# Kernel tuning notes

Hardware: AMD Instinct MI355X
Metric: run time of the kernel (lower is better)

The kernel has to match this reference:

```python
import jax, jax.numpy as jnp
import numpy as np

B, N_TOK, DIM, HEADS, FRAMES = 16, 1569, 768, 12, 8
HEAD_DIM = DIM // HEADS
N_SPACE = (N_TOK - 1) // FRAMES  # 196
EPS = 1e-6


def _ln(x, w, b):
    m = jnp.mean(x, axis=-1, keepdims=True)
    v = jnp.var(x, axis=-1, keepdims=True)
    return (x - m) * jax.lax.rsqrt(v + EPS) * w + b


def _sdpa(q, k, v):
    # q: [..., Sq, d], k/v: [..., Sk, d]
    s = jnp.einsum('...qd,...kd->...qk', q, k) * (HEAD_DIM ** -0.5)
    return jnp.einsum('...qk,...kd->...qd', jax.nn.softmax(s, axis=-1), v)


def _divided_attn(x, w_qkv, b_qkv, w_proj, b_proj, mode):
    # Faithful translation of DividedAttention.forward
    Bb, N, D = x.shape
    h, d, f = HEADS, HEAD_DIM, FRAMES
    n = (N - 1) // f
    qkv = x @ w_qkv + b_qkv                      # [B, N, 3D]
    q, k, v = jnp.split(qkv, 3, axis=-1)
    q, k, v = (t.reshape(Bb, N, h, d).transpose(0, 2, 1, 3) for t in (q, k, v))  # [B,h,N,d]
    # global cls-token attention over ALL tokens
    cls_out = _sdpa(q[:, :, :1], k, v)           # [B,h,1,d]
    # local tokens: split (f n) per einops pattern 'b (f n) d'
    q_, k_, v_ = (t[:, :, 1:].reshape(Bb, h, f, n, d) for t in (q, k, v))
    if mode == 'time':
        # '(b n) f d': batch over spatial positions, attend over frames
        q_, k_, v_ = (t.transpose(0, 1, 3, 2, 4) for t in (q_, k_, v_))  # [B,h,n,f,d]
        r = n
    else:
        # '(b f) n d': batch over frames, attend over spatial positions
        r = f
    cls_k = jnp.broadcast_to(k[:, :, None, :1], (Bb, h, r, 1, d))
    cls_v = jnp.broadcast_to(v[:, :, None, :1], (Bb, h, r, 1, d))
    out = _sdpa(q_,
                jnp.concatenate([cls_k, k_], axis=3),
                jnp.concatenate([cls_v, v_], axis=3))   # [B,h,r,seq,d]
    if mode == 'time':
        out = out.transpose(0, 1, 3, 2, 4)       # back to [B,h,f,n,d]
    out = out.reshape(Bb, h, N - 1, d)
    out = jnp.concatenate([cls_out, out], axis=2)          # [B,h,N,d]
    out = out.transpose(0, 2, 1, 3).reshape(Bb, N, D)      # 'b n (h d)'
    return out @ w_proj + b_proj


def setup_inputs() -> dict:
    key = jax.random.key(0)
    ks = jax.random.split(key, 8)
    s = 0.02
    return {
        'x': jax.random.normal(ks[0], (B, N_TOK, DIM), jnp.float32),
        'norm1_w': jnp.ones((DIM,), jnp.float32),
        'norm1_b': jnp.zeros((DIM,), jnp.float32),
        'norm2_w': jnp.ones((DIM,), jnp.float32),
        'norm2_b': jnp.zeros((DIM,), jnp.float32),
        'norm3_w': jnp.ones((DIM,), jnp.float32),
        'norm3_b': jnp.zeros((DIM,), jnp.float32),
        'time_qkv_w': jax.random.normal(ks[1], (DIM, 3 * DIM), jnp.float32) * s,
        'time_qkv_b': jnp.zeros((3 * DIM,), jnp.float32),
        'time_proj_w': jax.random.normal(ks[2], (DIM, DIM), jnp.float32) * s,
        'time_proj_b': jnp.zeros((DIM,), jnp.float32),
        'space_qkv_w': jax.random.normal(ks[3], (DIM, 3 * DIM), jnp.float32) * s,
        'space_qkv_b': jnp.zeros((3 * DIM,), jnp.float32),
        'space_proj_w': jax.random.normal(ks[4], (DIM, DIM), jnp.float32) * s,
        'space_proj_b': jnp.zeros((DIM,), jnp.float32),
        'mlp_w1': jax.random.normal(ks[5], (DIM, 4 * DIM), jnp.float32) * s,
        'mlp_b1': jnp.zeros((4 * DIM,), jnp.float32),
        'mlp_w2': jax.random.normal(ks[6], (4 * DIM, DIM), jnp.float32) * s,
        'mlp_b2': jnp.zeros((DIM,), jnp.float32),
    }


def reference(x, norm1_w, norm1_b, norm2_w, norm2_b, norm3_w, norm3_b,
              time_qkv_w, time_qkv_b, time_proj_w, time_proj_b,
              space_qkv_w, space_qkv_b, space_proj_w, space_proj_b,
              mlp_w1, mlp_b1, mlp_w2, mlp_b2):
    # DividedSpaceTimeBlock.forward
    t = _divided_attn(_ln(x, norm3_w, norm3_b),
                      time_qkv_w, time_qkv_b, time_proj_w, time_proj_b, 'time')
    x = x + t
    s = _divided_attn(_ln(x, norm1_w, norm1_b),
                      space_qkv_w, space_qkv_b, space_proj_w, space_proj_b, 'space')
    x = x + s
    h = jax.nn.gelu(_ln(x, norm2_w, norm2_b) @ mlp_w1 + mlp_b1)
    return x + h @ mlp_w2 + mlp_b2
```

## Files before the change

kernel.cpp:

```cpp
#include <hip/hip_runtime.h>
#include <cstdint>
#include <cstddef>

typedef unsigned short u16;
typedef __attribute__((ext_vector_type(8))) short short8;
typedef __attribute__((ext_vector_type(4))) float f32x4;

#define BB 16
#define NT 1569
#define DIM 768
#define NH 12
#define HD 64
#define FR 8
#define NS 196
#define MROWS (BB*NT)
#define NKEY 197

__device__ __forceinline__ float bf2f(u16 h) {
    return __uint_as_float(((unsigned int)h) << 16);
}
__device__ __forceinline__ u16 f2bf(float f) {
    unsigned int u = __float_as_uint(f);
    u += 0x7fff + ((u >> 16) & 1);
    return (u16)(u >> 16);
}

__global__ __launch_bounds__(256) void ln_kernel(const float* __restrict__ x,
        const float* __restrict__ w, const float* __restrict__ b,
        u16* __restrict__ out) {
    int row = blockIdx.x;
    size_t base = (size_t)row * DIM;
    int tid = threadIdx.x;
    float v0 = x[base + tid];
    float v1 = x[base + tid + 256];
    float v2 = x[base + tid + 512];
    float s = v0 + v1 + v2;
    float q = v0*v0 + v1*v1 + v2*v2;
    #pragma unroll
    for (int o = 32; o >= 1; o >>= 1) {
        s += __shfl_xor(s, o, 64);
        q += __shfl_xor(q, o, 64);
    }
    __shared__ float rs[4], rq[4];
    int wave = tid >> 6, lane = tid & 63;
    if (lane == 0) { rs[wave] = s; rq[wave] = q; }
    __syncthreads();
    float S = rs[0]+rs[1]+rs[2]+rs[3];
    float Q = rq[0]+rq[1]+rq[2]+rq[3];
    float mean = S * (1.0f/DIM);
    float var  = Q * (1.0f/DIM) - mean*mean;
    float inv  = rsqrtf(var + 1e-6f);
    out[base+tid]     = f2bf((v0-mean)*inv*w[tid]     + b[tid]);
    out[base+tid+256] = f2bf((v1-mean)*inv*w[tid+256] + b[tid+256]);
    out[base+tid+512] = f2bf((v2-mean)*inv*w[tid+512] + b[tid+512]);
}

__global__ __launch_bounds__(256) void wconv_kernel(const float* __restrict__ in,
        u16* __restrict__ out, int K, int N) {
    __shared__ float tile[32][33];
    int n0 = blockIdx.x * 32, k0 = blockIdx.y * 32;
    int tx = threadIdx.x & 31, ty = threadIdx.x >> 5;
    #pragma unroll
    for (int i = 0; i < 32; i += 8)
        tile[ty+i][tx] = in[(size_t)(k0+ty+i)*N + n0+tx];
    __syncthreads();
    #pragma unroll
    for (int i = 0; i < 32; i += 8)
        out[(size_t)(n0+ty+i)*K + k0+tx] = f2bf(tile[tx][ty+i]);
}

template<int EPI, bool OBF>
__global__ __launch_bounds__(256) void gemm_kernel(
        const u16* __restrict__ A, const u16* __restrict__ BT,
        const float* __restrict__ bias, const float* __restrict__ resid,
        void* __restrict__ Cout, int M, int N, int K) {
    __shared__ u16 lsA[128*40];
    __shared__ u16 lsB[128*40];
    int tid = threadIdx.x;
    int row0 = blockIdx.x * 128, col0 = blockIdx.y * 128;
    int wave = tid >> 6, lane = tid & 63;
    int wm = (wave >> 1) * 64, wn = (wave & 1) * 64;
    int lrow = lane & 15, quad = lane >> 4;
    f32x4 acc[4][4] = {};
    for (int k0 = 0; k0 < K; k0 += 32) {
        #pragma unroll
        for (int i = 0; i < 2; ++i) {
            int c = tid + i*256;
            int r = c >> 2, c8 = (c & 3) * 8;
            int gr = row0 + r; if (gr > M-1) gr = M-1;
            *(short8*)&lsA[r*40 + c8] = *(const short8*)(A + (size_t)gr*K + k0 + c8);
            *(short8*)&lsB[r*40 + c8] = *(const short8*)(BT + (size_t)(col0+r)*K + k0 + c8);
        }
        __syncthreads();
        short8 af[4], bfr[4];
        #pragma unroll
        for (int t = 0; t < 4; ++t)
            af[t] = *(const short8*)&lsA[(wm + t*16 + lrow)*40 + quad*8];
        #pragma unroll
        for (int t = 0; t < 4; ++t)
            bfr[t] = *(const short8*)&lsB[(wn + t*16 + lrow)*40 + quad*8];
        #pragma unroll
        for (int i = 0; i < 4; ++i)
            #pragma unroll
            for (int j = 0; j < 4; ++j)
                acc[i][j] = __builtin_amdgcn_mfma_f32_16x16x32_bf16(af[i], bfr[j], acc[i][j], 0, 0, 0);
        __syncthreads();
    }
    #pragma unroll
    for (int i = 0; i < 4; ++i) {
      #pragma unroll
      for (int j = 0; j < 4; ++j) {
        int gn = col0 + wn + j*16 + lrow;
        float bv = bias[gn];
        #pragma unroll
        for (int r = 0; r < 4; ++r) {
            int gm = row0 + wm + i*16 + quad*4 + r;
            if (gm < M) {
                float v = acc[i][j][r] + bv;
                if (EPI == 1) v += resid[(size_t)gm*N + gn];
                if (EPI == 2) {
                    float z = 0.7978845608028654f*(v + 0.044715f*v*v*v);
                    float t = 1.0f - 2.0f/(__expf(2.0f*z) + 1.0f);
                    v = 0.5f*v*(1.0f + t);
                }
                if (OBF) ((u16*)Cout)[(size_t)gm*N + gn] = f2bf(v);
                else     ((float*)Cout)[(size_t)gm*N + gn] = v;
            }
        }
      }
    }
}

__global__ __launch_bounds__(256) void attn_cls_kernel(const u16* __restrict__ qkv,
        u16* __restrict__ out) {
    __shared__ float s[NT];
    __shared__ float qf[64];
    __shared__ float part[4][64];
    __shared__ float red[4];
    int b = blockIdx.x / NH, h = blockIdx.x % NH;
    size_t base = ((size_t)b*NT)*(3*DIM) + h*HD;
    int tid = threadIdx.x;
    if (tid < 64) qf[tid] = bf2f(qkv[base + tid]);
    __syncthreads();
    float lmax = -1e30f;
    for (int t = tid; t < NT; t += 256) {
        const u16* kp = qkv + base + (size_t)t*(3*DIM) + DIM;
        float a0=0,a1=0,a2=0,a3=0;
        #pragma unroll
        for (int d = 0; d < 64; d += 4) {
            a0 += qf[d]  *bf2f(kp[d]);
            a1 += qf[d+1]*bf2f(kp[d+1]);
            a2 += qf[d+2]*bf2f(kp[d+2]);
            a3 += qf[d+3]*bf2f(kp[d+3]);
        }
        float sc = (a0+a1+a2+a3)*0.125f;
        s[t] = sc;
        lmax = fmaxf(lmax, sc);
    }
    #pragma unroll
    for (int o = 32; o >= 1; o >>= 1) lmax = fmaxf(lmax, __shfl_xor(lmax, o, 64));
    if ((tid&63) == 0) red[tid>>6] = lmax;
    __syncthreads();
    float m = fmaxf(fmaxf(red[0],red[1]), fmaxf(red[2],red[3]));
    float lsum = 0.f;
    for (int t = tid; t < NT; t += 256) { float e = __expf(s[t]-m); s[t] = e; lsum += e; }
    #pragma unroll
    for (int o = 32; o >= 1; o >>= 1) lsum += __shfl_xor(lsum, o, 64);
    __syncthreads();
    if ((tid&63) == 0) red[tid>>6] = lsum;
    __syncthreads();
    float inv = 1.0f/(red[0]+red[1]+red[2]+red[3]);
    int d = tid & 63, g = tid >> 6;
    float a = 0.f;
    for (int t = g; t < NT; t += 4)
        a += s[t]*bf2f(qkv[base + (size_t)t*(3*DIM) + 2*DIM + d]);
    part[g][d] = a;
    __syncthreads();
    if (tid < 64) {
        float o = (part[0][tid]+part[1][tid]+part[2][tid]+part[3][tid])*inv;
        out[((size_t)b*NT)*DIM + h*HD + tid] = f2bf(o);
    }
}

__global__ __launch_bounds__(256) void attn_time_kernel(const u16* __restrict__ qkv,
        u16* __restrict__ out) {
    __shared__ float qs[8][68], ks[9][68], vs[9][68];
    __shared__ float pr[8][12];
    int bid = blockIdx.x;
    int n = bid % NS; int rem = bid / NS; int h = rem % NH; int b = rem / NH;
    size_t base = ((size_t)b*NT)*(3*DIM) + h*HD;
    int tid = threadIdx.x;
    for (int idx = tid; idx < 512; idx += 256) {
        int f = idx >> 6, d = idx & 63;
        int tok = 1 + f*NS + n;
        size_t p = base + (size_t)tok*(3*DIM) + d;
        qs[f][d]   = bf2f(qkv[p]);
        ks[f+1][d] = bf2f(qkv[p + DIM]);
        vs[f+1][d] = bf2f(qkv[p + 2*DIM]);
    }
    if (tid < 64) {
        ks[0][tid] = bf2f(qkv[base + DIM + tid]);
        vs[0][tid] = bf2f(qkv[base + 2*DIM + tid]);
    }
    __syncthreads();
    if (tid < 72) {
        int fq = tid / 9, kk = tid % 9;
        float a0=0,a1=0,a2=0,a3=0;
        #pragma unroll
        for (int d = 0; d < 64; d += 4) {
            a0 += qs[fq][d]  *ks[kk][d];
            a1 += qs[fq][d+1]*ks[kk][d+1];
            a2 += qs[fq][d+2]*ks[kk][d+2];
            a3 += qs[fq][d+3]*ks[kk][d+3];
        }
        pr[fq][kk] = (a0+a1+a2+a3)*0.125f;
    }
    __syncthreads();
    if (tid < 8) {
        float m = -1e30f;
        #pragma unroll
        for (int kk = 0; kk < 9; ++kk) m = fmaxf(m, pr[tid][kk]);
        float sum = 0.f;
        #pragma unroll
        for (int kk = 0; kk < 9; ++kk) { float e = __expf(pr[tid][kk]-m); pr[tid][kk] = e; sum += e; }
        float inv = 1.0f/sum;
        #pragma unroll
        for (int kk = 0; kk < 9; ++kk) pr[tid][kk] *= inv;
    }
    __syncthreads();
    for (int idx = tid; idx < 512; idx += 256) {
        int fq = idx >> 6, d = idx & 63;
        float a = 0.f;
        #pragma unroll
        for (int kk = 0; kk < 9; ++kk) a += pr[fq][kk]*vs[kk][d];
        int tok = 1 + fq*NS + n;
        out[((size_t)b*NT + tok)*DIM + h*HD + d] = f2bf(a);
    }
}

#define VSTR 232
__global__ __launch_bounds__(256, 2) void attn_space_kernel(const u16* __restrict__ qkv,
        u16* __restrict__ out) {
    __shared__ u16 VT[64*VSTR];
    __shared__ u16 Ps[4][16*VSTR];
    int bid = blockIdx.x;
    int b = bid / (NH*FR); int rem = bid % (NH*FR); int h = rem / FR; int f = rem % FR;
    size_t base = ((size_t)b*NT)*(3*DIM) + (size_t)h*HD;
    int tid = threadIdx.x;
    int wave = tid >> 6, lane = tid & 63;
    int cb = lane & 15, quad = lane >> 4;

    for (int idx = tid; idx < NKEY*64; idx += 256) {
        int d = idx / NKEY, key = idx - d*NKEY;
        int tok = (key == 0) ? 0 : (1 + f*NS + key - 1);
        VT[d*VSTR + key] = qkv[base + (size_t)tok*(3*DIM) + 2*DIM + d];
    }
    for (int idx = tid; idx < 64*(VSTR-NKEY); idx += 256) {
        int d = idx / (VSTR-NKEY), c = idx - d*(VSTR-NKEY);
        VT[d*VSTR + NKEY + c] = 0;
    }
    for (int idx = tid; idx < 4*16*(VSTR-208); idx += 256) {
        int r = idx / (VSTR-208), c = idx - r*(VSTR-208);
        ((u16*)Ps)[r*VSTR + 208 + c] = 0;
    }
    __syncthreads();

    for (int qt = wave; qt < 13; qt += 4) {
        int q0 = qt*16;
        int qrow = q0 + cb; if (qrow > 195) qrow = 195;
        const u16* qp = qkv + base + (size_t)(1 + f*NS + qrow)*(3*DIM);
        short8 a0 = *(const short8*)(qp + quad*8);
        short8 a1 = *(const short8*)(qp + 32 + quad*8);
        f32x4 sacc[13];
        #pragma unroll
        for (int kt = 0; kt < 13; ++kt) {
            int key = kt*16 + cb; if (key > 196) key = 196;
            int ktok = (key == 0) ? 0 : (1 + f*NS + key - 1);
            const u16* kp = qkv + base + (size_t)ktok*(3*DIM) + DIM;
            short8 b0 = *(const short8*)(kp + quad*8);
            short8 b1 = *(const short8*)(kp + 32 + quad*8);
            f32x4 z = {0.f, 0.f, 0.f, 0.f};
            z = __builtin_amdgcn_mfma_f32_16x16x32_bf16(a0, b0, z, 0, 0, 0);
            z = __builtin_amdgcn_mfma_f32_16x16x32_bf16(a1, b1, z, 0, 0, 0);
            sacc[kt] = z;
        }
        bool last_ok = (cb < 5);
        float mx[4] = {-1e30f, -1e30f, -1e30f, -1e30f};
        #pragma unroll
        for (int kt = 0; kt < 13; ++kt) {
            bool ok = (kt < 12) || last_ok;
            #pragma unroll
            for (int r = 0; r < 4; ++r) {
                float v = sacc[kt][r] * 0.125f;
                sacc[kt][r] = v;
                if (ok) mx[r] = fmaxf(mx[r], v);
            }
        }
        #pragma unroll
        for (int off = 1; off < 16; off <<= 1)
            #pragma unroll
            for (int r = 0; r < 4; ++r)
                mx[r] = fmaxf(mx[r], __shfl_xor(mx[r], off, 64));
        float sum[4] = {0.f, 0.f, 0.f, 0.f};
        u16* prow = &Ps[wave][0];
        #pragma unroll
        for (int kt = 0; kt < 13; ++kt) {
            bool ok = (kt < 12) || last_ok;
            #pragma unroll
            for (int r = 0; r < 4; ++r) {
                float e = ok ? __expf(sacc[kt][r] - mx[r]) : 0.f;
                sum[r] += e;
                prow[(quad*4 + r)*VSTR + kt*16 + cb] = f2bf(e);
            }
        }
        #pragma unroll
        for (int off = 1; off < 16; off <<= 1)
            #pragma unroll
            for (int r = 0; r < 4; ++r)
                sum[r] += __shfl_xor(sum[r], off, 64);
        short8 pf[7];
        #pragma unroll
        for (int ks = 0; ks < 7; ++ks)
            pf[ks] = *(const short8*)&Ps[wave][cb*VSTR + ks*32 + quad*8];
        f32x4 oacc[4];
        #pragma unroll
        for (int nt = 0; nt < 4; ++nt) {
            f32x4 z = {0.f, 0.f, 0.f, 0.f};
            #pragma unroll
            for (int ks = 0; ks < 7; ++ks) {
                short8 vf = *(const short8*)&VT[(nt*16 + cb)*VSTR + ks*32 + quad*8];
                z = __builtin_amdgcn_mfma_f32_16x16x32_bf16(pf[ks], vf, z, 0, 0, 0);
            }
            oacc[nt] = z;
        }
        float inv[4];
        #pragma unroll
        for (int r = 0; r < 4; ++r) inv[r] = 1.0f / sum[r];
        #pragma unroll
        for (int r = 0; r < 4; ++r) {
            int qr = q0 + quad*4 + r;
            if (qr < 196) {
                size_t orow = ((size_t)b*NT + 1 + (size_t)f*NS + qr)*DIM + (size_t)h*HD;
                #pragma unroll
                for (int nt = 0; nt < 4; ++nt)
                    out[orow + nt*16 + cb] = f2bf(oacc[nt][r] * inv[r]);
            }
        }
    }
}

extern "C" void kernel_launch(void* const* d_in, const int* in_sizes, int n_in,
                              void* d_out, int out_size, void* d_ws, size_t ws_size,
                              hipStream_t stream) {
    const float* x          = (const float*)d_in[0];
    const float* norm1_w    = (const float*)d_in[1];
    const float* norm1_b    = (const float*)d_in[2];
    const float* norm2_w    = (const float*)d_in[3];
    const float* norm2_b    = (const float*)d_in[4];
    const float* norm3_w    = (const float*)d_in[5];
    const float* norm3_b    = (const float*)d_in[6];
    const float* t_qkv_w    = (const float*)d_in[7];
    const float* t_qkv_b    = (const float*)d_in[8];
    const float* t_proj_w   = (const float*)d_in[9];
    const float* t_proj_b   = (const float*)d_in[10];
    const float* s_qkv_w    = (const float*)d_in[11];
    const float* s_qkv_b    = (const float*)d_in[12];
    const float* s_proj_w   = (const float*)d_in[13];
    const float* s_proj_b   = (const float*)d_in[14];
    const float* mlp_w1     = (const float*)d_in[15];
    const float* mlp_b1     = (const float*)d_in[16];
    const float* mlp_w2     = (const float*)d_in[17];
    const float* mlp_b2     = (const float*)d_in[18];
    float* out = (float*)d_out;

    char* ws = (char*)d_ws;
    const size_t M = MROWS;
    u16*  qkv  = (u16*)(ws);
    u16*  attn = (u16*)(ws + M*2304*2);
    u16*  hbuf = (u16*)(ws);
    u16*  xn   = (u16*)(ws + M*3072*2);
    float* x1  = (float*)(ws + M*3072*2 + M*768*2);
    char* wsp  = ws + M*3072*2 + M*768*2 + M*768*4;
    u16* wqT_t = (u16*)(wsp);                 wsp += 2304*768*2;
    u16* wqT_s = (u16*)(wsp);                 wsp += 2304*768*2;
    u16* wpT_t = (u16*)(wsp);                 wsp += 768*768*2;
    u16* wpT_s = (u16*)(wsp);                 wsp += 768*768*2;
    u16* w1T   = (u16*)(wsp);                 wsp += 3072*768*2;
    u16* w2T   = (u16*)(wsp);

    wconv_kernel<<<dim3(2304/32, 768/32), 256, 0, stream>>>(t_qkv_w, wqT_t, 768, 2304);
    wconv_kernel<<<dim3(2304/32, 768/32), 256, 0, stream>>>(s_qkv_w, wqT_s, 768, 2304);
    wconv_kernel<<<dim3(768/32, 768/32), 256, 0, stream>>>(t_proj_w, wpT_t, 768, 768);
    wconv_kernel<<<dim3(768/32, 768/32), 256, 0, stream>>>(s_proj_w, wpT_s, 768, 768);
    wconv_kernel<<<dim3(3072/32, 768/32), 256, 0, stream>>>(mlp_w1, w1T, 768, 3072);
    wconv_kernel<<<dim3(768/32, 3072/32), 256, 0, stream>>>(mlp_w2, w2T, 3072, 768);

    const int GM = (MROWS + 127) / 128;

    ln_kernel<<<MROWS, 256, 0, stream>>>(x, norm3_w, norm3_b, xn);
    gemm_kernel<0, true ><<<dim3(GM, 2304/128), 256, 0, stream>>>(xn, wqT_t, t_qkv_b, nullptr, qkv, MROWS, 2304, 768);
    attn_cls_kernel <<<BB*NH, 256, 0, stream>>>(qkv, attn);
    attn_time_kernel<<<BB*NH*NS, 256, 0, stream>>>(qkv, attn);
    gemm_kernel<1, false><<<dim3(GM, 768/128), 256, 0, stream>>>(attn, wpT_t, t_proj_b, x, x1, MROWS, 768, 768);

    ln_kernel<<<MROWS, 256, 0, stream>>>(x1, norm1_w, norm1_b, xn);
    gemm_kernel<0, true ><<<dim3(GM, 2304/128), 256, 0, stream>>>(xn, wqT_s, s_qkv_b, nullptr, qkv, MROWS, 2304, 768);
    attn_cls_kernel  <<<BB*NH, 256, 0, stream>>>(qkv, attn);
    attn_space_kernel<<<BB*NH*FR, 256, 0, stream>>>(qkv, attn);
    gemm_kernel<1, false><<<dim3(GM, 768/128), 256, 0, stream>>>(attn, wpT_s, s_proj_b, x1, out, MROWS, 768, 768);

    ln_kernel<<<MROWS, 256, 0, stream>>>(out, norm2_w, norm2_b, xn);
    gemm_kernel<2, true ><<<dim3(GM, 3072/128), 256, 0, stream>>>(xn, w1T, mlp_b1, nullptr, hbuf, MROWS, 3072, 768);
    gemm_kernel<1, false><<<dim3(GM, 768/128), 256, 0, stream>>>(hbuf, w2T, mlp_b2, out, out, MROWS, 768, 3072);
}
```

Baseline: 1.745 ms.

## Use direct global-to-LDS loads, grouped tile swizzle, and bf16 intermediate residual

GEMM tiles are now loaded with global_load_lds, which writes straight into unpadded shared memory and skips the staging pass through registers. Blocks are remapped with a grouped M-major ordering to improve L2 reuse of the weight and activation tiles. The intermediate residual x1 is stored as bf16 instead of fp32, which halves its traffic but adds a rounding step to the residual stream. Dropping the LDS padding may cause bank conflicts when the MFMA fragments are read.

```diff
diff --git a/kernel.cpp b/kernel.cpp
--- a/kernel.cpp
+++ b/kernel.cpp
@@ -24,16 +24,27 @@
     u += 0x7fff + ((u >> 16) & 1);
     return (u16)(u >> 16);
 }
-
-__global__ __launch_bounds__(256) void ln_kernel(const float* __restrict__ x,
+__device__ __forceinline__ void gload_lds16(const u16* g, u16* l) {
+    __builtin_amdgcn_global_load_lds(
+        (const __attribute__((address_space(1))) void*)g,
+        (__attribute__((address_space(3))) void*)l, 16, 0, 0);
+}
+
+template<bool IBF>
+__global__ __launch_bounds__(256) void ln_kernel(const void* __restrict__ xin,
         const float* __restrict__ w, const float* __restrict__ b,
         u16* __restrict__ out) {
     int row = blockIdx.x;
     size_t base = (size_t)row * DIM;
     int tid = threadIdx.x;
-    float v0 = x[base + tid];
-    float v1 = x[base + tid + 256];
-    float v2 = x[base + tid + 512];
+    float v0, v1, v2;
+    if (IBF) {
+        const u16* x = (const u16*)xin;
+        v0 = bf2f(x[base + tid]); v1 = bf2f(x[base + tid + 256]); v2 = bf2f(x[base + tid + 512]);
+    } else {
+        const float* x = (const float*)xin;
+        v0 = x[base + tid]; v1 = x[base + tid + 256]; v2 = x[base + tid + 512];
+    }
     float s = v0 + v1 + v2;
     float q = v0*v0 + v1*v1 + v2*v2;
     #pragma unroll
@@ -69,36 +80,54 @@
         out[(size_t)(n0+ty+i)*K + k0+tx] = f2bf(tile[tx][ty+i]);
 }
 
-template<int EPI, bool OBF>
+template<int EPI, bool OBF, bool RBF>
 __global__ __launch_bounds__(256) void gemm_kernel(
         const u16* __restrict__ A, const u16* __restrict__ BT,
-        const float* __restrict__ bias, const float* __restrict__ resid,
-        void* __restrict__ Cout, int M, int N, int K) {
-    __shared__ u16 lsA[128*40];
-    __shared__ u16 lsB[128*40];
+        const float* __restrict__ bias, const void* __restrict__ resid,
+        void* __restrict__ Cout, int M, int N, int K, int num_m, int num_n) {
+    __shared__ u16 lsA[128*32];
+    __shared__ u16 lsB[128*32];
+    const int GRP = 16;
+    int pid = blockIdx.x;
+    int gsz = GRP * num_n;
+    int gid = pid / gsz;
+    int rem = pid - gid*gsz;
+    int m0b = gid * GRP;
+    int msz = num_m - m0b; if (msz > GRP) msz = GRP;
+    int pm = m0b + rem % msz;
+    int pn = rem / msz;
+    int row0 = pm * 128, col0 = pn * 128;
     int tid = threadIdx.x;
-    int row0 = blockIdx.x * 128, col0 = blockIdx.y * 128;
     int wave = tid >> 6, lane = tid & 63;
     int wm = (wave >> 1) * 64, wn = (wave & 1) * 64;
     int lrow = lane & 15, quad = lane >> 4;
+    int srow = lane >> 2, scol = (lane & 3) * 8;
+    const u16* gAp[2]; const u16* gBp[2];
+    u16* lA[2]; u16* lB[2];
+    #pragma unroll
+    for (int i = 0; i < 2; ++i) {
+        int r = wave*32 + i*16 + srow;
+        int gr = row0 + r; if (gr > M-1) gr = M-1;
+        gAp[i] = A  + (size_t)gr*K + scol;
+        gBp[i] = BT + (size_t)(col0 + r)*K + scol;
+        lA[i] = &lsA[(wave*32 + i*16)*32];
+        lB[i] = &lsB[(wave*32 + i*16)*32];
+    }
     f32x4 acc[4][4] = {};
     for (int k0 = 0; k0 < K; k0 += 32) {
         #pragma unroll
         for (int i = 0; i < 2; ++i) {
-            int c = tid + i*256;
-            int r = c >> 2, c8 = (c & 3) * 8;
-            int gr = row0 + r; if (gr > M-1) gr = M-1;
-            *(short8*)&lsA[r*40 + c8] = *(const short8*)(A + (size_t)gr*K + k0 + c8);
-            *(short8*)&lsB[r*40 + c8] = *(const short8*)(BT + (size_t)(col0+r)*K + k0 + c8);
+            gload_lds16(gAp[i] + k0, lA[i]);
+            gload_lds16(gBp[i] + k0, lB[i]);
         }
         __syncthreads();
         short8 af[4], bfr[4];
         #pragma unroll
         for (int t = 0; t < 4; ++t)
-            af[t] = *(const short8*)&lsA[(wm + t*16 + lrow)*40 + quad*8];
+            af[t] = *(const short8*)&lsA[(wm + t*16 + lrow)*32 + quad*8];
         #pragma unroll
         for (int t = 0; t < 4; ++t)
-            bfr[t] = *(const short8*)&lsB[(wn + t*16 + lrow)*40 + quad*8];
+            bfr[t] = *(const short8*)&lsB[(wn + t*16 + lrow)*32 + quad*8];
         #pragma unroll
         for (int i = 0; i < 4; ++i)
             #pragma unroll
@@ -117,7 +146,10 @@
             int gm = row0 + wm + i*16 + quad*4 + r;
             if (gm < M) {
                 float v = acc[i][j][r] + bv;
-                if (EPI == 1) v += resid[(size_t)gm*N + gn];
+                if (EPI == 1) {
+                    size_t ridx = (size_t)gm*N + gn;
+                    v += RBF ? bf2f(((const u16*)resid)[ridx]) : ((const float*)resid)[ridx];
+                }
                 if (EPI == 2) {
                     float z = 0.7978845608028654f*(v + 0.044715f*v*v*v);
                     float t = 1.0f - 2.0f/(__expf(2.0f*z) + 1.0f);
@@ -379,7 +411,7 @@
     u16*  attn = (u16*)(ws + M*2304*2);
     u16*  hbuf = (u16*)(ws);
     u16*  xn   = (u16*)(ws + M*3072*2);
-    float* x1  = (float*)(ws + M*3072*2 + M*768*2);
+    u16*  x1   = (u16*)(ws + M*3072*2 + M*768*2);
     char* wsp  = ws + M*3072*2 + M*768*2 + M*768*4;
     u16* wqT_t = (u16*)(wsp);                 wsp += 2304*768*2;
     u16* wqT_s = (u16*)(wsp);                 wsp += 2304*768*2;
@@ -397,19 +429,19 @@
 
     const int GM = (MROWS + 127) / 128;
 
-    ln_kernel<<<MROWS, 256, 0, stream>>>(x, norm3_w, norm3_b, xn);
-    gemm_kernel<0, true ><<<dim3(GM, 2304/128), 256, 0, stream>>>(xn, wqT_t, t_qkv_b, nullptr, qkv, MROWS, 2304, 768);
+    ln_kernel<false><<<MROWS, 256, 0, stream>>>(x, norm3_w, norm3_b, xn);
+    gemm_kernel<0, true, false><<<GM*(2304/128), 256, 0, stream>>>(xn, wqT_t, t_qkv_b, nullptr, qkv, MROWS, 2304, 768, GM, 2304/128);
     attn_cls_kernel <<<BB*NH, 256, 0, stream>>>(qkv, attn);
     attn_time_kernel<<<BB*NH*NS, 256, 0, stream>>>(qkv, attn);
-    gemm_kernel<1, false><<<dim3(GM, 768/128), 256, 0, stream>>>(attn, wpT_t, t_proj_b, x, x1, MROWS, 768, 768);
-
-    ln_kernel<<<MROWS, 256, 0, stream>>>(x1, norm1_w, norm1_b, xn);
-    gemm_kernel<0, true ><<<dim3(GM, 2304/128), 256, 0, stream>>>(xn, wqT_s, s_qkv_b, nullptr, qkv, MROWS, 2304, 768);
+    gemm_kernel<1, true, false><<<GM*(768/128), 256, 0, stream>>>(attn, wpT_t, t_proj_b, x, x1, MROWS, 768, 768, GM, 768/128);
+
+    ln_kernel<true><<<MROWS, 256, 0, stream>>>(x1, norm1_w, norm1_b, xn);
+    gemm_kernel<0, true, false><<<GM*(2304/128), 256, 0, stream>>>(xn, wqT_s, s_qkv_b, nullptr, qkv, MROWS, 2304, 768, GM, 2304/128);
     attn_cls_kernel  <<<BB*NH, 256, 0, stream>>>(qkv, attn);
     attn_space_kernel<<<BB*NH*FR, 256, 0, stream>>>(qkv, attn);
-    gemm_kernel<1, false><<<dim3(GM, 768/128), 256, 0, stream>>>(attn, wpT_s, s_proj_b, x1, out, MROWS, 768, 768);
-
-    ln_kernel<<<MROWS, 256, 0, stream>>>(out, norm2_w, norm2_b, xn);
-    gemm_kernel<2, true ><<<dim3(GM, 3072/128), 256, 0, stream>>>(xn, w1T, mlp_b1, nullptr, hbuf, MROWS, 3072, 768);
-    gemm_kernel<1, false><<<dim3(GM, 768/128), 256, 0, stream>>>(hbuf, w2T, mlp_b2, out, out, MROWS, 768, 3072);
-}
+    gemm_kernel<1, false, true><<<GM*(768/128), 256, 0, stream>>>(attn, wpT_s, s_proj_b, x1, out, MROWS, 768, 768, GM, 768/128);
+
+    ln_kernel<false><<<MROWS, 256, 0, stream>>>(out, norm2_w, norm2_b, xn);
+    gemm_kernel<2, true, false><<<GM*(3072/128), 256, 0, stream>>>(xn, w1T, mlp_b1, nullptr, hbuf, MROWS, 3072, 768, GM, 3072/128);
+    gemm_kernel<1, false, false><<<GM*(768/128), 256, 0, stream>>>(hbuf, w2T, mlp_b2, out, out, MROWS, 768, 3072, GM, 768/128);
+}
```

Measured after the change: 1.560 ms. -10.6%, faster.
